# Kernel tuning notes

Measured on AMD Instinct MI355X. Metric: run time of the kernel, lower is better.

The kernel has to match this reference:

```python
import jax, jax.numpy as jnp
import numpy as np

VOCAB, D = 14848, 128

def setup_inputs() -> dict:
    key = jax.random.key(0)
    ks = jax.random.split(key, 7)
    x = jax.random.randint(ks[0], (65536, 32), 0, VOCAB, dtype=jnp.int32)
    emb = jax.random.normal(ks[1], (VOCAB, D), dtype=jnp.float32) * 0.05
    w2 = jax.random.normal(ks[2], (32, 128), dtype=jnp.float32) * (1.0 / np.sqrt(128))
    b2 = jax.random.normal(ks[3], (32,), dtype=jnp.float32) * 0.01
    w3 = jax.random.normal(ks[4], (32, 64), dtype=jnp.float32) * (1.0 / np.sqrt(64))
    b3 = jax.random.normal(ks[5], (32,), dtype=jnp.float32) * 0.01
    w4 = jax.random.normal(ks[6], (1, 64), dtype=jnp.float32) * (1.0 / np.sqrt(64))
    return {"x": x, "emb": emb, "w2": w2, "b2": b2, "w3": w3, "b3": b3, "w4": w4}

def reference(x, emb, w2, b2, w3, b3, w4):
    idx = x[..., :29]                      # [B, 29]
    h = emb[idx].sum(axis=-2)              # [B, 128] gather + sum accumulator
    h = jax.nn.relu(h)
    h = h @ w2.T + b2                      # [B, 32]
    h = jax.nn.relu(jnp.concatenate((h, -h), axis=-1))  # [B, 64]
    h = h @ w3.T + b3                      # [B, 32]
    h = jax.nn.relu(jnp.concatenate((h, -h), axis=-1))  # [B, 64]
    return h @ w4.T                        # [B, 1]
```

## Files before the change

### kernel.cpp

```cpp
#include <hip/hip_runtime.h>
#include <hip/hip_fp16.h>


#define STR 65

using h8 = __attribute__((ext_vector_type(8))) _Float16;
using h4 = __attribute__((ext_vector_type(4))) _Float16;

__device__ __forceinline__ float frelu(float v) { return v > 0.f ? v : 0.f; }

__global__ __launch_bounds__(256) void cvt_emb(const float* __restrict__ emb,
                                               _Float16* __restrict__ tab) {
    const int i = blockIdx.x * 256 + threadIdx.x;
    const float4 v = ((const float4*)emb)[i];
    h4 o;
    o[0] = (_Float16)v.x; o[1] = (_Float16)v.y;
    o[2] = (_Float16)v.z; o[3] = (_Float16)v.w;
    ((h4*)tab)[i] = o;
}

__global__ __launch_bounds__(256, 4) void nnue_fwd(
    const int* __restrict__ x, const _Float16* __restrict__ tab,
    const float* __restrict__ w2, const float* __restrict__ b2,
    const float* __restrict__ w3, const float* __restrict__ b3,
    const float* __restrict__ w4, float* __restrict__ out)
{
    __shared__ float lds[128 * STR];

    const int t    = threadIdx.x;
    const int lane = t & 63;
    const int g    = lane >> 4;
    const int sub  = lane & 15;
    const int row0 = blockIdx.x * 64;
    const int wave = __builtin_amdgcn_readfirstlane(t >> 6);

    for (int rr = 0; rr < 16; ++rr) {
        const int rloc = wave * 16 + rr;
        const int xv = x[(size_t)(row0 + rloc) * 32 + (lane & 31)];

        float acc[8] = {0.f, 0.f, 0.f, 0.f, 0.f, 0.f, 0.f, 0.f};
        #pragma unroll
        for (int jj = 0; jj < 7; ++jj) {
            const int idx = __shfl(xv, 4 * jj + g, 64);
            const h8 v = *((const h8*)(tab + (size_t)idx * 128) + sub);
            #pragma unroll
            for (int k = 0; k < 8; ++k) acc[k] += (float)v[k];
        }
        {
            const int idx = __shfl(xv, 28, 64);
            if (g == 0) {
                const h8 v = *((const h8*)(tab + (size_t)idx * 128) + sub);
                #pragma unroll
                for (int k = 0; k < 8; ++k) acc[k] += (float)v[k];
            }
        }
        #pragma unroll
        for (int k = 0; k < 8; ++k) {
            acc[k] += __shfl_xor(acc[k], 16, 64);
            acc[k] += __shfl_xor(acc[k], 32, 64);
        }
        const int d0 = 8 * sub + 2 * g;
        lds[(d0 + 0) * STR + rloc] = frelu(acc[2 * g + 0]);
        lds[(d0 + 1) * STR + rloc] = frelu(acc[2 * g + 1]);
    }
    __syncthreads();

    const int r  = lane;
    const int ob = __builtin_amdgcn_readfirstlane((t >> 6) * 8);

    float a2[8];
    #pragma unroll
    for (int oo = 0; oo < 8; ++oo) a2[oo] = b2[ob + oo];
    #pragma unroll 4
    for (int d = 0; d < 128; ++d) {
        const float hv = lds[d * STR + r];
        #pragma unroll
        for (int oo = 0; oo < 8; ++oo)
            a2[oo] = fmaf(hv, w2[(ob + oo) * 128 + d], a2[oo]);
    }
    __syncthreads();
    #pragma unroll
    for (int oo = 0; oo < 8; ++oo) lds[(ob + oo) * STR + r] = a2[oo];
    __syncthreads();

    float a3[8];
    #pragma unroll
    for (int oo = 0; oo < 8; ++oo) a3[oo] = b3[ob + oo];
    #pragma unroll 4
    for (int j = 0; j < 32; ++j) {
        const float v = lds[j * STR + r];
        const float p = frelu(v), n = frelu(-v);
        #pragma unroll
        for (int oo = 0; oo < 8; ++oo)
            a3[oo] = fmaf(p, w3[(ob + oo) * 64 + j],
                     fmaf(n, w3[(ob + oo) * 64 + 32 + j], a3[oo]));
    }
    #pragma unroll
    for (int oo = 0; oo < 8; ++oo) lds[(32 + ob + oo) * STR + r] = a3[oo];
    __syncthreads();

    if (t < 64) {
        float s = 0.f;
        #pragma unroll 4
        for (int j = 0; j < 32; ++j) {
            const float v = lds[(32 + j) * STR + t];
            s = fmaf(frelu(v), w4[j], fmaf(frelu(-v), w4[32 + j], s));
        }
        out[row0 + t] = s;
    }
}

extern "C" void kernel_launch(void* const* d_in, const int* in_sizes, int n_in,
                              void* d_out, int out_size, void* d_ws, size_t ws_size,
                              hipStream_t stream) {
    const int*   x   = (const int*)d_in[0];
    const float* emb = (const float*)d_in[1];
    const float* w2  = (const float*)d_in[2];
    const float* b2  = (const float*)d_in[3];
    const float* w3  = (const float*)d_in[4];
    const float* b3  = (const float*)d_in[5];
    const float* w4  = (const float*)d_in[6];
    float* out = (float*)d_out;

    _Float16* tab = (_Float16*)d_ws;

    const int emb_elems = in_sizes[1];
    const int n_rows    = in_sizes[0] / 32;

    hipLaunchKernelGGL(cvt_emb, dim3(emb_elems / 4 / 256), dim3(256), 0, stream,
                       emb, tab);
    hipLaunchKernelGGL(nnue_fwd, dim3(n_rows / 64), dim3(256), 0, stream,
                       x, tab, w2, b2, w3, b3, w4, out);
}
```

Baseline: 119.5 us.

## Accumulate gathers in packed fp16 and use fdot2 for the dense layers

The embedding gather now has each 16-lane group own a full row. Sums run in packed half2 across two alternating accumulators, which removes the cross-group shuffle reduction. Activations are stored in LDS as half2 pairs (relu(v), relu(-v)), and the MLP layers use fdot2 against fp16 weights packed by a new prep kernel. This halves LDS traffic and the FMA count, but fp16 accumulation of 29 terms and the fp16 weights reduce precision.

```diff
diff --git a/kernel.cpp b/kernel.cpp
--- a/kernel.cpp
+++ b/kernel.cpp
@@ -4,10 +4,20 @@
 
 #define STR 65
 
-using h8 = __attribute__((ext_vector_type(8))) _Float16;
-using h4 = __attribute__((ext_vector_type(4))) _Float16;
+using h2  = _Float16 __attribute__((ext_vector_type(2)));
+using h4  = _Float16 __attribute__((ext_vector_type(4)));
+using h8v = _Float16 __attribute__((ext_vector_type(8)));
+
+union H8 { h8v v; h2 h[4]; };
 
 __device__ __forceinline__ float frelu(float v) { return v > 0.f ? v : 0.f; }
+
+__device__ __forceinline__ h2 h2relu(h2 v) {
+    h2 r;
+    r[0] = v[0] > (_Float16)0 ? v[0] : (_Float16)0;
+    r[1] = v[1] > (_Float16)0 ? v[1] : (_Float16)0;
+    return r;
+}
 
 __global__ __launch_bounds__(256) void cvt_emb(const float* __restrict__ emb,
                                                _Float16* __restrict__ tab) {
@@ -19,13 +29,30 @@
     ((h4*)tab)[i] = o;
 }
 
+__global__ __launch_bounds__(256) void prep_w(
+    const float* __restrict__ w2, const float* __restrict__ w3,
+    const float* __restrict__ w4,
+    _Float16* __restrict__ w2p, h2* __restrict__ w3p, h2* __restrict__ w4p) {
+    const int i = threadIdx.x;
+    for (int e = i; e < 32 * 128; e += 256) w2p[e] = (_Float16)w2[e];
+    for (int p = i; p < 32 * 32; p += 256) {
+        const int o = p >> 5, j = p & 31;
+        h2 c; c[0] = (_Float16)w3[o * 64 + j]; c[1] = (_Float16)w3[o * 64 + 32 + j];
+        w3p[p] = c;
+    }
+    if (i < 32) {
+        h2 c; c[0] = (_Float16)w4[i]; c[1] = (_Float16)w4[32 + i];
+        w4p[i] = c;
+    }
+}
+
 __global__ __launch_bounds__(256, 4) void nnue_fwd(
     const int* __restrict__ x, const _Float16* __restrict__ tab,
-    const float* __restrict__ w2, const float* __restrict__ b2,
-    const float* __restrict__ w3, const float* __restrict__ b3,
-    const float* __restrict__ w4, float* __restrict__ out)
+    const h2* __restrict__ w2p, const float* __restrict__ b2,
+    const h2* __restrict__ w3p, const float* __restrict__ b3,
+    const h2* __restrict__ w4p, float* __restrict__ out)
 {
-    __shared__ float lds[128 * STR];
+    __shared__ h2 lds[64 * STR];
 
     const int t    = threadIdx.x;
     const int lane = t & 63;
@@ -34,34 +61,32 @@
     const int row0 = blockIdx.x * 64;
     const int wave = __builtin_amdgcn_readfirstlane(t >> 6);
 
-    for (int rr = 0; rr < 16; ++rr) {
-        const int rloc = wave * 16 + rr;
-        const int xv = x[(size_t)(row0 + rloc) * 32 + (lane & 31)];
+    for (int it = 0; it < 4; ++it) {
+        const int rb = wave * 16 + it * 4;
+        const int xv0 = x[(size_t)(row0 + rb + g) * 32 + sub];
+        const int xv1 = x[(size_t)(row0 + rb + g) * 32 + 16 + sub];
 
-        float acc[8] = {0.f, 0.f, 0.f, 0.f, 0.f, 0.f, 0.f, 0.f};
+        h2 accA[4] = {}, accB[4] = {};
         #pragma unroll
-        for (int jj = 0; jj < 7; ++jj) {
-            const int idx = __shfl(xv, 4 * jj + g, 64);
-            const h8 v = *((const h8*)(tab + (size_t)idx * 128) + sub);
-            #pragma unroll
-            for (int k = 0; k < 8; ++k) acc[k] += (float)v[k];
-        }
-        {
-            const int idx = __shfl(xv, 28, 64);
-            if (g == 0) {
-                const h8 v = *((const h8*)(tab + (size_t)idx * 128) + sub);
-                #pragma unroll
-                for (int k = 0; k < 8; ++k) acc[k] += (float)v[k];
+        for (int j = 0; j < 29; ++j) {
+            const int src = (lane & 48) | (j & 15);
+            const int idx = __shfl((j < 16) ? xv0 : xv1, src, 64);
+            H8 u;
+            u.v = *(const h8v*)((const char*)tab +
+                                (((unsigned)idx) << 8) + (sub << 4));
+            if (j & 1) {
+                accB[0] += u.h[0]; accB[1] += u.h[1];
+                accB[2] += u.h[2]; accB[3] += u.h[3];
+            } else {
+                accA[0] += u.h[0]; accA[1] += u.h[1];
+                accA[2] += u.h[2]; accA[3] += u.h[3];
             }
         }
         #pragma unroll
-        for (int k = 0; k < 8; ++k) {
-            acc[k] += __shfl_xor(acc[k], 16, 64);
-            acc[k] += __shfl_xor(acc[k], 32, 64);
+        for (int k = 0; k < 4; ++k) {
+            const h2 s = h2relu(accA[k] + accB[k]);
+            lds[(4 * sub + k) * STR + rb + g] = s;
         }
-        const int d0 = 8 * sub + 2 * g;
-        lds[(d0 + 0) * STR + rloc] = frelu(acc[2 * g + 0]);
-        lds[(d0 + 1) * STR + rloc] = frelu(acc[2 * g + 1]);
     }
     __syncthreads();
 
@@ -71,41 +96,45 @@
     float a2[8];
     #pragma unroll
     for (int oo = 0; oo < 8; ++oo) a2[oo] = b2[ob + oo];
-    #pragma unroll 4
-    for (int d = 0; d < 128; ++d) {
-        const float hv = lds[d * STR + r];
+    #pragma unroll 8
+    for (int pd = 0; pd < 64; ++pd) {
+        const h2 hp = lds[pd * STR + r];
         #pragma unroll
         for (int oo = 0; oo < 8; ++oo)
-            a2[oo] = fmaf(hv, w2[(ob + oo) * 128 + d], a2[oo]);
+            a2[oo] = __builtin_amdgcn_fdot2(hp, w2p[(ob + oo) * 64 + pd],
+                                            a2[oo], false);
     }
     __syncthreads();
     #pragma unroll
-    for (int oo = 0; oo < 8; ++oo) lds[(ob + oo) * STR + r] = a2[oo];
+    for (int oo = 0; oo < 8; ++oo) {
+        h2 c; c[0] = (_Float16)frelu(a2[oo]); c[1] = (_Float16)frelu(-a2[oo]);
+        lds[(ob + oo) * STR + r] = c;
+    }
     __syncthreads();
 
     float a3[8];
     #pragma unroll
     for (int oo = 0; oo < 8; ++oo) a3[oo] = b3[ob + oo];
-    #pragma unroll 4
+    #pragma unroll 8
     for (int j = 0; j < 32; ++j) {
-        const float v = lds[j * STR + r];
-        const float p = frelu(v), n = frelu(-v);
+        const h2 cp = lds[j * STR + r];
         #pragma unroll
         for (int oo = 0; oo < 8; ++oo)
-            a3[oo] = fmaf(p, w3[(ob + oo) * 64 + j],
-                     fmaf(n, w3[(ob + oo) * 64 + 32 + j], a3[oo]));
+            a3[oo] = __builtin_amdgcn_fdot2(cp, w3p[(ob + oo) * 32 + j],
+                                            a3[oo], false);
     }
     #pragma unroll
-    for (int oo = 0; oo < 8; ++oo) lds[(32 + ob + oo) * STR + r] = a3[oo];
+    for (int oo = 0; oo < 8; ++oo) {
+        h2 c; c[0] = (_Float16)frelu(a3[oo]); c[1] = (_Float16)frelu(-a3[oo]);
+        lds[(32 + ob + oo) * STR + r] = c;
+    }
     __syncthreads();
 
     if (t < 64) {
         float s = 0.f;
-        #pragma unroll 4
-        for (int j = 0; j < 32; ++j) {
-            const float v = lds[(32 + j) * STR + t];
-            s = fmaf(frelu(v), w4[j], fmaf(frelu(-v), w4[32 + j], s));
-        }
+        #pragma unroll
+        for (int j = 0; j < 32; ++j)
+            s = __builtin_amdgcn_fdot2(lds[(32 + j) * STR + t], w4p[j], s, false);
         out[row0 + t] = s;
     }
 }
@@ -122,13 +151,19 @@
     const float* w4  = (const float*)d_in[6];
     float* out = (float*)d_out;
 
-    _Float16* tab = (_Float16*)d_ws;
-
     const int emb_elems = in_sizes[1];
     const int n_rows    = in_sizes[0] / 32;
 
+    char* ws = (char*)d_ws;
+    _Float16* tab = (_Float16*)ws;
+    _Float16* w2p = (_Float16*)(ws + 3801088);
+    h2*       w3p = (h2*)(ws + 3801088 + 8192);
+    h2*       w4p = (h2*)(ws + 3801088 + 8192 + 4096);
+
     hipLaunchKernelGGL(cvt_emb, dim3(emb_elems / 4 / 256), dim3(256), 0, stream,
                        emb, tab);
+    hipLaunchKernelGGL(prep_w, dim3(1), dim3(256), 0, stream,
+                       w2, w3, w4, w2p, w3p, w4p);
     hipLaunchKernelGGL(nnue_fwd, dim3(n_rows / 64), dim3(256), 0, stream,
-                       x, tab, w2, b2, w3, b3, w4, out);
+                       x, tab, (const h2*)w2p, b2, w3p, b3, w4p, out);
 }
```

Result: faster. 106.4 us (-11.0%).
